# Performance work log

Measured on AMD Instinct MI355X. Metric: run time of the kernel, lower is better.

Reference implementation:

```python
import jax, jax.numpy as jnp
import numpy as np

H = 12            # heads
NB_FEATURES = 256 # Performer random features
EPS = 1e-4        # performer_pytorch softmax_kernel eps


def _gaussian_orthogonal_matrix(nb_rows, nb_cols, rng):
    # performer_pytorch gaussian_orthogonal_random_matrix, scaling=0
    nb_full = nb_rows // nb_cols
    blocks = []
    for _ in range(nb_full):
        q, _ = np.linalg.qr(rng.standard_normal((nb_cols, nb_cols)))
        blocks.append(q.T)
    rem = nb_rows - nb_full * nb_cols
    if rem > 0:
        q, _ = np.linalg.qr(rng.standard_normal((nb_cols, nb_cols)))
        blocks.append(q.T[:rem])
    M = np.concatenate(blocks, axis=0)
    multiplier = np.linalg.norm(rng.standard_normal((nb_rows, nb_cols)), axis=1)
    return (multiplier[:, None] * M).astype(np.float32)


def setup_inputs() -> dict:
    key = jax.random.key(0)
    ks = jax.random.split(key, 10)
    B, N, D = 8, 2048, 768
    s = D ** -0.5  # keep activations O(1) so exp() in FAVOR+ is stable
    inp = {
        "x": jax.random.normal(ks[0], (B, N, D), jnp.float32),
        "Wq": jax.random.normal(ks[1], (D, D), jnp.float32) * s,
        "bq": jnp.zeros((D,), jnp.float32),
        "Wk": jax.random.normal(ks[2], (D, D), jnp.float32) * s,
        "bk": jnp.zeros((D,), jnp.float32),
        "Wv": jax.random.normal(ks[3], (D, D), jnp.float32) * s,
        "bv": jnp.zeros((D,), jnp.float32),
        "Wo": jax.random.normal(ks[4], (D, D), jnp.float32) * s,
        "bo": jnp.zeros((D,), jnp.float32),
        "proj": jnp.asarray(_gaussian_orthogonal_matrix(NB_FEATURES, D // H, np.random.default_rng(0))),
    }
    return inp


def _softmax_kernel(x, proj, is_query):
    # x: [b,h,n,d], proj: [m,d] -> phi(x): [b,h,n,m]
    d = x.shape[-1]
    data_normalizer = d ** -0.25
    ratio = proj.shape[0] ** -0.5
    xp = jnp.einsum('bhnd,md->bhnm', x * data_normalizer, proj)
    diag = jnp.sum(x * x, axis=-1, keepdims=True) * 0.5 * (data_normalizer ** 2)
    if is_query:
        m = jax.lax.stop_gradient(jnp.max(xp, axis=-1, keepdims=True))
    else:
        m = jax.lax.stop_gradient(jnp.max(xp, axis=(-1, -2), keepdims=True))
    return ratio * (jnp.exp(xp - diag - m) + EPS)


def reference(x, Wq, bq, Wk, bk, Wv, bv, Wo, bo, proj):
    b, n, dim = x.shape
    d = dim // H
    # qkv projections, split into heads: [b,h,n,d]
    q = (x @ Wq.T + bq).reshape(b, n, H, d).transpose(0, 2, 1, 3)
    k = (x @ Wk.T + bk).reshape(b, n, H, d).transpose(0, 2, 1, 3)
    v = (x @ Wv.T + bv).reshape(b, n, H, d).transpose(0, 2, 1, 3)
    # FAVOR+ feature maps: [b,h,n,m]
    qp = _softmax_kernel(q, proj, True)
    kp = _softmax_kernel(k, proj, False)
    # non-causal linear attention
    k_sum = kp.sum(axis=2)                                  # [b,h,m]
    D_inv = 1.0 / jnp.einsum('bhnm,bhm->bhn', qp, k_sum)    # [b,h,n]
    ctx = jnp.einsum('bhnm,bhnd->bhmd', kp, v)              # [b,h,m,d]
    out = jnp.einsum('bhmd,bhnm,bhn->bhnd', ctx, qp, D_inv)
    out = out.transpose(0, 2, 1, 3).reshape(b, n, dim)
    return out @ Wo.T + bo
```

## Files before the change

kernel.cpp:

```cpp
#include <hip/hip_runtime.h>
#include <stdint.h>

typedef unsigned short u16;
typedef unsigned int u32;
typedef __attribute__((ext_vector_type(8))) short short8;
typedef __attribute__((ext_vector_type(4))) float floatx4;

#define HN 12
#define DH 64
#define DM 768
#define NS 2048
#define NB 8
#define MF 256
#define BN (NB*NS)
#define BH (NB*HN)

#define NRM 0.35355339059327373f
#define RATIO 0.0625f
#define EPSV 1e-4f

__device__ __forceinline__ float b2f(u32 u){ union{u32 i; float f;} x; x.i=u<<16; return x.f; }
__device__ __forceinline__ u32 f2b(float v){ union{float f; u32 u;} x; x.f=v; return (x.u + 0x7FFFu + ((x.u>>16)&1u))>>16; }
__device__ __forceinline__ u32 fkey(float v){ union{float f; u32 u;} x; x.f=v; return (x.u&0x80000000u)? ~x.u : (x.u|0x80000000u); }
__device__ __forceinline__ float funkey(u32 k){ union{u32 u; float f;} x; x.u=(k&0x80000000u)? (k^0x80000000u) : ~k; return x.f; }
__device__ __forceinline__ void bld8(uint4 r, float s, float* f){
  f[0]=b2f(r.x&0xffffu)*s; f[1]=b2f(r.x>>16)*s;
  f[2]=b2f(r.y&0xffffu)*s; f[3]=b2f(r.y>>16)*s;
  f[4]=b2f(r.z&0xffffu)*s; f[5]=b2f(r.z>>16)*s;
  f[6]=b2f(r.w&0xffffu)*s; f[7]=b2f(r.w>>16)*s;
}
__device__ __forceinline__ void load8(const void* base, size_t idx, int isf32, float s, float* f){
  if(isf32){
    const float* p=(const float*)base + idx;
    const float4 u=((const float4*)p)[0], v=((const float4*)p)[1];
    f[0]=u.x*s; f[1]=u.y*s; f[2]=u.z*s; f[3]=u.w*s;
    f[4]=v.x*s; f[5]=v.y*s; f[6]=v.z*s; f[7]=v.w*s;
  }else{
    uint4 r=*(const uint4*)((const u16*)base+idx);
    bld8(r,s,f);
  }
}
__device__ __forceinline__ float ld1(const void* base, int idx, int isf32){
  return isf32 ? ((const float*)base)[idx] : b2f((u32)((const u16*)base)[idx]);
}
__device__ __forceinline__ void gl16(const void* g, void* l){
  __builtin_amdgcn_global_load_lds(
    (const __attribute__((address_space(1))) u32*)g,
    (__attribute__((address_space(3))) u32*)l, 16, 0, 0);
}

__global__ __launch_bounds__(64) void k_detect(const u16* __restrict__ x, int* __restrict__ flag)
{
  __shared__ int w[64], z[64];
  const int t=threadIdx.x;
  int wild=0, zero=0;
  for(int i=t;i<256;i+=64){
    u32 u=(u32)x[2*i];
    u32 e=(u>>7)&0xFFu;
    if(e>=0x90u) wild++;
    if((u&0x7FFFu)==0u) zero++;
  }
  w[t]=wild; z[t]=zero; __syncthreads();
  if(t==0){
    int W=0,Z=0;
    for(int i=0;i<64;++i){W+=w[i];Z+=z[i];}
    flag[0]=(W>16||Z>200)?1:0;
  }
}

__global__ __launch_bounds__(256) void k_cvtw(const void* __restrict__ Wq,
    const void* __restrict__ Wk, const void* __restrict__ Wv, const void* __restrict__ Wo,
    u16* __restrict__ wb, u16* __restrict__ wob, const int* __restrict__ flagp)
{
  const int isf32=*flagp;
  const size_t WSZ=(size_t)DM*DM;
  size_t idx=((size_t)blockIdx.x*256+threadIdx.x)*8;
  const void* src; size_t off; u16* dst;
  if(idx<3*WSZ){ int w=(int)(idx/WSZ); src=(w==0)?Wq:((w==1)?Wk:Wv); off=idx-(size_t)w*WSZ; dst=wb+idx; }
  else { src=Wo; off=idx-3*WSZ; dst=wob+off; }
  if(isf32){
    const float* p=(const float*)src+off;
    float4 u=((const float4*)p)[0], v=((const float4*)p)[1];
    uint4 st;
    st.x=f2b(u.x)|(f2b(u.y)<<16); st.y=f2b(u.z)|(f2b(u.w)<<16);
    st.z=f2b(v.x)|(f2b(v.y)<<16); st.w=f2b(v.z)|(f2b(v.w)<<16);
    *(uint4*)dst=st;
  }else{
    *(uint4*)dst=*(const uint4*)((const u16*)src+off);
  }
}

__global__ __launch_bounds__(256) void k_cvtp(const void* __restrict__ proj,
    u16* __restrict__ pn, const int* __restrict__ flagp)
{
  const int isf32=*flagp;
  const size_t idx=((size_t)blockIdx.x*256+threadIdx.x)*8;
  float pf[8];
  load8(proj, idx, isf32, NRM, pf);
  uint4 st;
  st.x=f2b(pf[0])|(f2b(pf[1])<<16); st.y=f2b(pf[2])|(f2b(pf[3])<<16);
  st.z=f2b(pf[4])|(f2b(pf[5])<<16); st.w=f2b(pf[6])|(f2b(pf[7])<<16);
  *(uint4*)(pn+idx)=st;
}

__global__ __launch_bounds__(256) void k_cvtx(const void* __restrict__ x,
    u16* __restrict__ xb, const int* __restrict__ flagp)
{
  const int isf32=*flagp;
  const size_t idx=((size_t)blockIdx.x*256+threadIdx.x)*8;
  float f[8];
  load8(x, idx, isf32, 1.0f, f);
  uint4 st;
  st.x=f2b(f[0])|(f2b(f[1])<<16); st.y=f2b(f[2])|(f2b(f[3])<<16);
  st.z=f2b(f[4])|(f2b(f[5])<<16); st.w=f2b(f[6])|(f2b(f[7])<<16);
  *(uint4*)(xb+idx)=st;
}

__global__ __launch_bounds__(256) void k_diag(const u16* __restrict__ src, float* __restrict__ dk)
{
  const size_t row=(size_t)blockIdx.x*256+threadIdx.x;
  const u16* p=src+row*DH;
  float s=0.f;
#pragma unroll
  for(int c=0;c<DH;c+=8){
    uint4 r=*(const uint4*)(p+c);
    float f[8]; bld8(r,1.0f,f);
#pragma unroll
    for(int j=0;j<8;++j) s+=f[j]*f[j];
  }
  dk[row]=0.5f*NRM*NRM*s;
}

__device__ __forceinline__ void gemm_epilogue(const floatx4 acc[4][4], int mode, int oflag,
    int m0, int n0, int l, int wr4, int wc4,
    const void* bias0, const void* bias1, const void* bias2,
    u16* q, u16* k, u16* v, void* outv)
{
  const int rbase=(l>>4)*4, cl=l&15;
  if(mode==0){
    const int which=n0/DM;
    const void* bias=(which==0)?bias0:((which==1)?bias1:bias2);
    u16* outp=(which==0)?q:((which==1)?k:v);
    const int cb=n0-which*DM;
#pragma unroll
    for(int j=0;j<4;++j){
      const int col=cb+(wc4+j)*16+cl;
      const int h=col>>6, dd=col&63;
      const float bb=ld1(bias,col,oflag);
#pragma unroll
      for(int i=0;i<4;++i){
#pragma unroll
        for(int r=0;r<4;++r){
          const int grow=m0+(wr4+i)*16+rbase+r;
          const int b_=grow>>11, n=grow&2047;
          const u16 val=(u16)f2b(acc[i][j][r]+bb);
          if(which==2) outp[((size_t)(b_*HN+h)*DH+dd)*NS + n]=val;
          else         outp[((size_t)((b_*HN+h)*NS+n))*DH + dd]=val;
        }
      }
    }
  }else{
#pragma unroll
    for(int j=0;j<4;++j){
      const int col=n0+(wc4+j)*16+cl;
      const float bb=ld1(bias0,col,oflag);
#pragma unroll
      for(int i=0;i<4;++i){
#pragma unroll
        for(int r=0;r<4;++r){
          const int grow=m0+(wr4+i)*16+rbase+r;
          const float val=acc[i][j][r]+bb;
          if(oflag) ((float*)outv)[(size_t)grow*DM+col]=val;
          else      ((u16*)outv)[(size_t)grow*DM+col]=(u16)f2b(val);
        }
      }
    }
  }
}

__global__ __launch_bounds__(256) void k_gemm2(const u16* __restrict__ A16,
    const u16* __restrict__ B16,
    const void* __restrict__ bias0, const void* __restrict__ bias1, const void* __restrict__ bias2,
    u16* __restrict__ q, u16* __restrict__ k, u16* __restrict__ v,
    void* __restrict__ outv, const int* __restrict__ flagp, const int mode)
{
  __shared__ short At[16*512];
  __shared__ short Bt[16*512];
  const int oflag=*flagp;
  const int t=threadIdx.x, l=t&63, w=t>>6;
  const int m0=blockIdx.x*128, n0=blockIdx.y*128;
  const int wr4=(w>>1)*4, wc4=(w&1)*4;
  const int srow=l&15, skg=l>>4;
  floatx4 acc[4][4]={};
  for(int k0=0;k0<DM;k0+=64){
    __syncthreads();
#pragma unroll
    for(int s=0;s<4;++s){
      const int bi=w*4+s, rb=bi>>1, kh=bi&1;
      const int kc=k0+kh*32+skg*8;
      gl16(A16 + (size_t)(m0+rb*16+srow)*DM + kc, &At[bi*512]);
      gl16(B16 + (size_t)(n0+rb*16+srow)*DM + kc, &Bt[bi*512]);
    }
    __syncthreads();
#pragma unroll
    for(int kh=0;kh<2;++kh){
      short8 af[4], bf[4];
#pragma unroll
      for(int i=0;i<4;++i) af[i]=*(short8*)&At[((wr4+i)*2+kh)*512+l*8];
#pragma unroll
      for(int j=0;j<4;++j) bf[j]=*(short8*)&Bt[((wc4+j)*2+kh)*512+l*8];
#pragma unroll
      for(int i=0;i<4;++i)
#pragma unroll
        for(int j=0;j<4;++j)
          acc[i][j]=__builtin_amdgcn_mfma_f32_16x16x32_bf16(af[i],bf[j],acc[i][j],0,0,0);
    }
  }
  gemm_epilogue(acc,mode,oflag,m0,n0,l,wr4,wc4,bias0,bias1,bias2,q,k,v,outv);
}

__global__ __launch_bounds__(256) void k_gemm_f(const void* __restrict__ Araw,
    const u16* __restrict__ B16,
    const void* __restrict__ bias0, const void* __restrict__ bias1, const void* __restrict__ bias2,
    u16* __restrict__ q, u16* __restrict__ k, u16* __restrict__ v,
    void* __restrict__ outv, const int* __restrict__ flagp, const int mode)
{
  __shared__ short At[16*512];
  __shared__ short Bt[16*512];
  const int oflag=*flagp;
  const int isf32=(mode==0)?oflag:0;
  const int t=threadIdx.x, l=t&63, w=t>>6;
  const int m0=blockIdx.x*128, n0=blockIdx.y*128;
  const int wr4=(w>>1)*4, wc4=(w&1)*4;
  const int srow=l&15, skg=l>>4;
  floatx4 acc[4][4]={};
  for(int k0=0;k0<DM;k0+=64){
    __syncthreads();
#pragma unroll
    for(int s=0;s<4;++s){
      const int bi=w*4+s, rb=bi>>1, kh=bi&1;
      const int kc=k0+kh*32+skg*8;
      uint4 va;
      if(isf32){
        const float* ap=(const float*)Araw + (size_t)(m0+rb*16+srow)*DM + kc;
        float4 u=((const float4*)ap)[0], vv=((const float4*)ap)[1];
        va.x=f2b(u.x)|(f2b(u.y)<<16);  va.y=f2b(u.z)|(f2b(u.w)<<16);
        va.z=f2b(vv.x)|(f2b(vv.y)<<16); va.w=f2b(vv.z)|(f2b(vv.w)<<16);
      }else{
        va=*(const uint4*)((const u16*)Araw + (size_t)(m0+rb*16+srow)*DM + kc);
      }
      const uint4 vb=*(const uint4*)(B16 + (size_t)(n0+rb*16+srow)*DM + kc);
      *(uint4*)&At[bi*512+l*8]=va;
      *(uint4*)&Bt[bi*512+l*8]=vb;
    }
    __syncthreads();
#pragma unroll
    for(int kh=0;kh<2;++kh){
      short8 af[4], bf[4];
#pragma unroll
      for(int i=0;i<4;++i) af[i]=*(short8*)&At[((wr4+i)*2+kh)*512+l*8];
#pragma unroll
      for(int j=0;j<4;++j) bf[j]=*(short8*)&Bt[((wc4+j)*2+kh)*512+l*8];
#pragma unroll
      for(int i=0;i<4;++i)
#pragma unroll
        for(int j=0;j<4;++j)
          acc[i][j]=__builtin_amdgcn_mfma_f32_16x16x32_bf16(af[i],bf[j],acc[i][j],0,0,0);
    }
  }
  gemm_epilogue(acc,mode,oflag,m0,n0,l,wr4,wc4,bias0,bias1,bias2,q,k,v,outv);
}

#define G9OFF(s,u) (((s)*24+(u))*512)
#define G9STA(kt,s) do{ \
  const size_t g_=(size_t)(kt)*32; \
  gl16(Ar0+g_, &LD[G9OFF(s,w)]); \
  gl16(Ar0+(size_t)128*768+g_, &LD[G9OFF(s,8+w)]); \
  gl16(Br0+g_, &LD[G9OFF(s,16+w)]); \
}while(0)
#define G9LD(s) do{ \
  _Pragma("unroll") for(int i_=0;i_<4;++i_) a[i_]=*(short8*)&LD[G9OFF(s,wr4+i_)+l*8]; \
  _Pragma("unroll") for(int j_=0;j_<4;++j_) b[j_]=*(short8*)&LD[G9OFF(s,16+wc4+j_)+l*8]; \
}while(0)
#define G9MM do{ _Pragma("unroll") for(int i_=0;i_<4;++i_){ \
  _Pragma("unroll") for(int j_=0;j_<4;++j_) \
    acc[i_][j_]=__builtin_amdgcn_mfma_f32_16x16x32_bf16(a[i_],b[j_],acc[i_][j_],0,0,0); } }while(0)
#define FEN asm volatile("" ::: "memory")
#define BARR do{ FEN; __builtin_amdgcn_s_barrier(); FEN; }while(0)
#define WV3 asm volatile("s_waitcnt vmcnt(3)" ::: "memory")
#define WV0 asm volatile("s_waitcnt vmcnt(0)" ::: "memory")
#define WL0 do{ asm volatile("s_waitcnt lgkmcnt(0)" ::: "memory"); __builtin_amdgcn_sched_barrier(0); }while(0)
#define G9PH(kt,s,SST,WST) do{ G9LD(s); SST; WST; BARR; WL0; \
  __builtin_amdgcn_s_setprio(1); G9MM; __builtin_amdgcn_s_setprio(0); BARR; }while(0)

__global__ __launch_bounds__(512,4) void k_gemm9(const u16* __restrict__ A16,
    const u16* __restrict__ B16,
    const void* __restrict__ bias0, const void* __restrict__ bias1, const void* __restrict__ bias2,
    u16* __restrict__ q, u16* __restrict__ k, u16* __restrict__ v,
    void* __restrict__ outv, const int* __restrict__ flagp, const int mode,
    float* __restrict__ dq_, float* __restrict__ dk_)
{
  __shared__ short LD[3*24*512];
  const int oflag=*flagp;
  const int t=threadIdx.x, l=t&63, w=t>>6;
  const int wr=w>>1, wc=w&1;
  const int wr4=wr*4, wc4=wc*4;
  const int lrow=l&15, lk8=(l>>4)*8;
  int bid = blockIdx.y*gridDim.x + blockIdx.x;
  const int nwg = gridDim.x*gridDim.y;
  const int nN  = gridDim.y;
  bid = (bid&7)*(nwg>>3) + (bid>>3);
  const int mi = bid/nN;
  const int m0 = mi*256;
  const int n0 = (bid - mi*nN)*128;

  const u16* Ar0 = A16 + (size_t)(m0 + w*16 + lrow)*768 + lk8;
  const u16* Br0 = B16 + (size_t)(n0 + w*16 + lrow)*768 + lk8;
  floatx4 acc[4][4]={};
  short8 a[4], b[4];

  G9STA(0,0); G9STA(1,1);
  WV3; BARR;

  for(int it=0; it<7; ++it){
    const int kt=3*it;
    G9PH(kt+0,0, G9STA(kt+2,2), WV3);
    G9PH(kt+1,1, G9STA(kt+3,0), WV3);
    G9PH(kt+2,2, G9STA(kt+4,1), WV3);
  }
  G9PH(21,0, G9STA(23,2), WV3);
  G9PH(22,1, (void)0, WV0);
  G9PH(23,2, (void)0, (void)0);

  char* LB=(char*)LD;
  const int cl=l&15, q4=l>>4;
  const int wrm=wr*64, wcn=wc*64;
  if(mode==0){
    const int which=n0/DM;
    const int cb0=n0-which*DM;
    const int hb=cb0>>6;
    const void* bias=(which==0)?bias0:((which==1)?bias1:bias2);
    u16* outp=(which==0)?q:((which==1)?k:v);
    if(which==2){
#pragma unroll
      for(int j=0;j<4;++j){
        const int col=wcn+j*16+cl;
        const float bb=ld1(bias,cb0+col,oflag);
        const int X=(col&7)<<4;
#pragma unroll
        for(int i=0;i<4;++i){
          const int rowb=wrm+i*16+q4*4;
          uint2 pk;
          pk.x=f2b(acc[i][j][0]+bb)|(f2b(acc[i][j][1]+bb)<<16);
          pk.y=f2b(acc[i][j][2]+bb)|(f2b(acc[i][j][3]+bb)<<16);
          *(uint2*)(LB + col*512 + ((rowb*2)^X)) = pk;
        }
      }
      __syncthreads();
      const int b_=m0>>11, nbase=m0&2047;
#pragma unroll
      for(int s8=0;s8<8;++s8){
        const int c=s8*512+t;
        const int col=c>>5, off=(c&31)*16;
        const uint4 d4=*(const uint4*)(LB + col*512 + (off^((col&7)<<4)));
        const int h=hb+(col>>6), dd=col&63;
        *(uint4*)&outp[((size_t)(b_*HN+h)*DH+dd)*NS + nbase + (off>>1)]=d4;
      }
    } else {
      float bb4[4];
#pragma unroll
      for(int j=0;j<4;++j) bb4[j]=ld1(bias, cb0+wcn+j*16+cl, oflag);
      float* dptr=(which==0)? dq_ : dk_;
#pragma unroll
      for(int i=0;i<4;++i){
#pragma unroll
        for(int r=0;r<4;++r){
          const int row=wrm+i*16+q4*4+r;
          const int X=(row&7)<<4;
          float s=0.f;
#pragma unroll
          for(int j=0;j<4;++j){
            const int col=wcn+j*16+cl;
            const u16 hv=(u16)f2b(acc[i][j][r]+bb4[j]);
            *(u16*)(LB + row*256 + ((col*2)^X)) = hv;
            const float fv=b2f(hv);
            s+=fv*fv;
          }
          s+=__shfl_xor(s,1,64); s+=__shfl_xor(s,2,64);
          s+=__shfl_xor(s,4,64); s+=__shfl_xor(s,8,64);
          if(cl==0){
            const int grow=m0+row, b_=grow>>11, n=grow&2047;
            dptr[(size_t)(b_*HN + hb + wc)*NS + n]=0.5f*NRM*NRM*s;
          }
        }
      }
      __syncthreads();
#pragma unroll
      for(int s8=0;s8<8;++s8){
        const int c=s8*512+t;
        const int row=c>>4, off=(c&15)*16;
        const uint4 d4=*(const uint4*)(LB + row*256 + (off^((row&7)<<4)));
        const int grow=m0+row, b_=grow>>11, n=grow&2047;
        *(uint4*)&outp[((size_t)((b_*HN+hb+(off>>7))*NS+n))*DH + ((off>>1)&63)]=d4;
      }
    }
  } else {
    if(oflag){
#pragma unroll
      for(int p=0;p<2;++p){
        if((wr>>1)==p){
          const int rl0=(wr&1)*64;
#pragma unroll
          for(int j=0;j<4;++j){
            const int col=wcn+j*16+cl;
            const float bb=ld1(bias0,n0+col,oflag);
#pragma unroll
            for(int i=0;i<4;++i){
#pragma unroll
              for(int r=0;r<4;++r){
                const int rl=rl0+i*16+q4*4+r;
                *(float*)(LB + rl*512 + ((col*4)^((rl&7)<<4))) = acc[i][j][r]+bb;
              }
            }
          }
        }
        __syncthreads();
#pragma unroll
        for(int s8=0;s8<8;++s8){
          const int c=s8*512+t;
          const int rl=c>>5, off=(c&31)*16;
          const uint4 d4=*(const uint4*)(LB + rl*512 + (off^((rl&7)<<4)));
          const size_t grow=(size_t)m0+p*128+rl;
          *(uint4*)((char*)outv + (grow*DM+n0)*4 + off)=d4;
        }
        __syncthreads();
      }
    } else {
#pragma unroll
      for(int j=0;j<4;++j){
        const int col=wcn+j*16+cl;
        const float bb=ld1(bias0,n0+col,oflag);
#pragma unroll
        for(int i=0;i<4;++i){
#pragma unroll
          for(int r=0;r<4;++r){
            const int row=wrm+i*16+q4*4+r;
            *(u16*)(LB + row*256 + ((col*2)^((row&7)<<4))) = (u16)f2b(acc[i][j][r]+bb);
          }
        }
      }
      __syncthreads();
#pragma unroll
      for(int s8=0;s8<8;++s8){
        const int c=s8*512+t;
        const int row=c>>4, off=(c&15)*16;
        const uint4 d4=*(const uint4*)(LB + row*256 + (off^((row&7)<<4)));
        *(uint4*)((u16*)outv + (size_t)(m0+row)*DM + n0 + (off>>1))=d4;
      }
    }
  }
}

__global__ __launch_bounds__(256) void k_xpk2(const u16* __restrict__ kb,
    const u16* __restrict__ pn, u32* __restrict__ kmax)
{
  __shared__ short Bt[32*512];
  __shared__ short At[8*512];
  __shared__ float red[256];
  const int t=threadIdx.x, l=t&63, w=t>>6;
  const int bh=blockIdx.y, nb0=blockIdx.x*256;
  for(int s=t;s<2048;s+=256){
    const int ub=s>>6, l2=s&63, mt=ub>>1, kh=ub&1;
    const int row=mt*16+(l2&15), kc=kh*32+(l2>>4)*8;
    *(uint4*)&Bt[ub*512+l2*8]=*(const uint4*)(pn + (size_t)row*DH + kc);
  }
  float vmax=-3.4e38f;
  for(int c=0;c<4;++c){
    const int n0=nb0+c*64;
    __syncthreads();
    for(int s=t;s<512;s+=256){
      const int ua=s>>6, l2=s&63, rb=ua>>1, kh=ua&1;
      const int n=n0+rb*16+(l2&15), kc=kh*32+(l2>>4)*8;
      *(uint4*)&At[ua*512+l2*8]=*(const uint4*)(kb + ((size_t)bh*NS+n)*DH + kc);
    }
    __syncthreads();
    const short8 af0=*(short8*)&At[(w*2+0)*512+l*8];
    const short8 af1=*(short8*)&At[(w*2+1)*512+l*8];
#pragma unroll
    for(int mt=0;mt<16;++mt){
      floatx4 a={};
      a=__builtin_amdgcn_mfma_f32_16x16x32_bf16(af0,*(short8*)&Bt[(mt*2+0)*512+l*8],a,0,0,0);
      a=__builtin_amdgcn_mfma_f32_16x16x32_bf16(af1,*(short8*)&Bt[(mt*2+1)*512+l*8],a,0,0,0);
      vmax=fmaxf(vmax,fmaxf(fmaxf(a[0],a[1]),fmaxf(a[2],a[3])));
    }
  }
  red[t]=vmax; __syncthreads();
  for(int s=128;s>0;s>>=1){ if(t<s) red[t]=fmaxf(red[t],red[t+s]); __syncthreads(); }
  if(t==0) atomicMax(kmax+bh, fkey(red[0]));
}

__global__ __launch_bounds__(256) void k_ctx2(const u16* __restrict__ kb,
    const u16* __restrict__ vT, const u16* __restrict__ pn,
    const float* __restrict__ dkbuf, const u32* __restrict__ kmax,
    float* __restrict__ ctxT, float* __restrict__ ksum)
{
  __shared__ short Bt[32*512];
  __shared__ u16   Ks[256*72];
  __shared__ short AtV[8*512];
  __shared__ float dg[64];
  const int t=threadIdx.x, l=t&63, w=t>>6;
  const int split=blockIdx.x, bh=blockIdx.y;
  for(int s=t;s<2048;s+=256){
    const int ub=s>>6, l2=s&63, mt=ub>>1, kh=ub&1;
    const int row=mt*16+(l2&15), kc=kh*32+(l2>>4)*8;
    *(uint4*)&Bt[ub*512+l2*8]=*(const uint4*)(pn + (size_t)row*DH + kc);
  }
  const float kM=funkey(kmax[bh]);
  float ksr=0.f;
  floatx4 acc2[4][4]={};
  for(int c=0;c<8;++c){
    const int n0=split*512+c*64;
    __syncthreads();
    for(int s=t;s<512;s+=256){
      const int ua=s>>6, l2=s&63, rb=ua>>1, kh=ua&1;
      const int n=n0+rb*16+(l2&15), kc=kh*32+(l2>>4)*8;
      *(uint4*)&AtV[ua*512+l2*8]=*(const uint4*)(kb + ((size_t)bh*NS+n)*DH + kc);
    }
    if(t<64) dg[t]=dkbuf[(size_t)bh*NS+n0+t];
    __syncthreads();
    short8 af[4][2];
#pragma unroll
    for(int rb=0;rb<4;++rb){
      af[rb][0]=*(short8*)&AtV[(rb*2+0)*512+l*8];
      af[rb][1]=*(short8*)&AtV[(rb*2+1)*512+l*8];
    }
    float dgl[16];
#pragma unroll
    for(int rb=0;rb<4;++rb)
#pragma unroll
      for(int r=0;r<4;++r) dgl[rb*4+r]=dg[rb*16+(l>>4)*4+r];
#pragma unroll
    for(int ml=0;ml<4;++ml){
      const int mt=w*4+ml;
      const short8 bf0=*(short8*)&Bt[(mt*2+0)*512+l*8];
      const short8 bf1=*(short8*)&Bt[(mt*2+1)*512+l*8];
      const int m=mt*16+(l&15);
#pragma unroll
      for(int rb=0;rb<4;++rb){
        floatx4 a={};
        a=__builtin_amdgcn_mfma_f32_16x16x32_bf16(af[rb][0],bf0,a,0,0,0);
        a=__builtin_amdgcn_mfma_f32_16x16x32_bf16(af[rb][1],bf1,a,0,0,0);
        const int nb=rb*16+(l>>4)*4;
        const float v0=RATIO*(__expf(a[0]-dgl[rb*4+0]-kM)+EPSV);
        const float v1=RATIO*(__expf(a[1]-dgl[rb*4+1]-kM)+EPSV);
        const float v2=RATIO*(__expf(a[2]-dgl[rb*4+2]-kM)+EPSV);
        const float v3=RATIO*(__expf(a[3]-dgl[rb*4+3]-kM)+EPSV);
        *(u32*)&Ks[m*72+nb]  =f2b(v0)|(f2b(v1)<<16);
        *(u32*)&Ks[m*72+nb+2]=f2b(v2)|(f2b(v3)<<16);
      }
    }
    __syncthreads();
    for(int s=t;s<512;s+=256){
      const int uv=s>>6, l2=s&63, dt=uv>>1, kh=uv&1;
      const int d=dt*16+(l2&15), nn=n0+kh*32+(l2>>4)*8;
      *(uint4*)&AtV[uv*512+l2*8]=*(const uint4*)(vT + ((size_t)bh*DH+d)*NS + nn);
    }
    {
      float s8=0.f;
#pragma unroll
      for(int j=0;j<8;++j){
        const uint4 kk=*(const uint4*)&Ks[t*72+j*8];
        s8+=b2f(kk.x&0xffffu)+b2f(kk.x>>16)+b2f(kk.y&0xffffu)+b2f(kk.y>>16)
           +b2f(kk.z&0xffffu)+b2f(kk.z>>16)+b2f(kk.w&0xffffu)+b2f(kk.w>>16);
      }
      ksr+=s8;
    }
    __syncthreads();
#pragma unroll
    for(int i=0;i<4;++i){
      const int row=(w*4+i)*16+(l&15);
      const short8 a0=*(short8*)&Ks[row*72 + 0*32+(l>>4)*8];
      const short8 a1=*(short8*)&Ks[row*72 + 1*32+(l>>4)*8];
#pragma unroll
      for(int dt=0;dt<4;++dt){
        acc2[i][dt]=__builtin_amdgcn_mfma_f32_16x16x32_bf16(a0,*(short8*)&AtV[(dt*2+0)*512+l*8],acc2[i][dt],0,0,0);
        acc2[i][dt]=__builtin_amdgcn_mfma_f32_16x16x32_bf16(a1,*(short8*)&AtV[(dt*2+1)*512+l*8],acc2[i][dt],0,0,0);
      }
    }
  }
#pragma unroll
  for(int i=0;i<4;++i){
#pragma unroll
    for(int dt=0;dt<4;++dt){
#pragma unroll
      for(int r=0;r<4;++r){
        const int m=(w*4+i)*16+(l>>4)*4+r;
        const int d=dt*16+(l&15);
        atomicAdd(&ctxT[((size_t)bh*DH+d)*MF+m], acc2[i][dt][r]);
      }
    }
  }
  atomicAdd(ksum+bh*MF+t, ksr);
}

__global__ __launch_bounds__(256,2) void k_ctx3(const u16* __restrict__ kb,
    const u16* __restrict__ vT, const u16* __restrict__ pn,
    const float* __restrict__ dkbuf, const u32* __restrict__ kmax,
    float* __restrict__ ctxP, float* __restrict__ ksumP)
{
  __shared__ __align__(16) char SM[66048];
  short* Ks=(short*)SM;
  short* Kb=(short*)(SM+32768);
  short* Vb=(short*)(SM+49152);
  float* dgb=(float*)(SM+65536);
  const int t=threadIdx.x, l=t&63, w=t>>6;
  const int split=blockIdx.x, bh=blockIdx.y;
  const int n00=split*512;
  const int lrow=l&15, lk8=(l>>4)*8;
  const u16* kbase = kb + (size_t)bh*NS*DH;
  const u16* vbase = vT + (size_t)bh*DH*NS;
  short8 bf[4][2];
#pragma unroll
  for(int ml=0;ml<4;++ml)
#pragma unroll
    for(int kh=0;kh<2;++kh)
      bf[ml][kh]=*(const short8*)(pn + (size_t)((w*4+ml)*16+lrow)*DH + kh*32 + lk8);
  const float kM=funkey(kmax[bh]);
  {
#pragma unroll
    for(int p=0;p<2;++p){
      const int u=w+4*p, rb=u>>1, kh=u&1;
      gl16(kbase + (size_t)(n00+rb*16+lrow)*DH + kh*32+lk8, &Kb[u*512]);
    }
#pragma unroll
    for(int p=0;p<2;++p){
      const int u=w+4*p, dt=u>>1, kh=u&1;
      gl16(vbase + (size_t)(dt*16+lrow)*NS + n00+kh*32+lk8, &Vb[u*512]);
    }
    if(t<64) dgb[t]=dkbuf[(size_t)bh*NS+n00+t];
  }
  __syncthreads();
  float ksr=0.f;
  floatx4 acc2[4][4]={};
  for(int c=0;c<8;++c){
    const int cur=c&1, nxt=cur^1;
    if(c<7){
      const int n1=n00+(c+1)*64;
#pragma unroll
      for(int p=0;p<2;++p){
        const int u=w+4*p, rb=u>>1, kh=u&1;
        gl16(kbase + (size_t)(n1+rb*16+lrow)*DH + kh*32+lk8, &Kb[nxt*4096+u*512]);
      }
#pragma unroll
      for(int p=0;p<2;++p){
        const int u=w+4*p, dt=u>>1, kh=u&1;
        gl16(vbase + (size_t)(dt*16+lrow)*NS + n1+kh*32+lk8, &Vb[nxt*4096+u*512]);
      }
    }
    float dgnv=0.f;
    if(c<7 && t<64) dgnv=dkbuf[(size_t)bh*NS+n00+(c+1)*64+t];
    short8 af[4][2];
#pragma unroll
    for(int rb=0;rb<4;++rb){
      af[rb][0]=*(short8*)&Kb[cur*4096+(rb*2+0)*512+l*8];
      af[rb][1]=*(short8*)&Kb[cur*4096+(rb*2+1)*512+l*8];
    }
    float dgl[16];
#pragma unroll
    for(int rb=0;rb<4;++rb){
      const float4 dv=*(const float4*)&dgb[cur*64+rb*16+(l>>4)*4];
      dgl[rb*4+0]=dv.x; dgl[rb*4+1]=dv.y; dgl[rb*4+2]=dv.z; dgl[rb*4+3]=dv.w;
    }
#pragma unroll
    for(int ml=0;ml<4;++ml){
      const int m=(w*4+ml)*16+lrow;
      char* krow=(char*)Ks + m*128;
      const int xr=(m&7)<<4;
#pragma unroll
      for(int rb=0;rb<4;++rb){
        floatx4 a={};
        a=__builtin_amdgcn_mfma_f32_16x16x32_bf16(af[rb][0],bf[ml][0],a,0,0,0);
        a=__builtin_amdgcn_mfma_f32_16x16x32_bf16(af[rb][1],bf[ml][1],a,0,0,0);
        const float v0=RATIO*(__expf(a[0]-dgl[rb*4+0]-kM)+EPSV);
        const float v1=RATIO*(__expf(a[1]-dgl[rb*4+1]-kM)+EPSV);
        const float v2=RATIO*(__expf(a[2]-dgl[rb*4+2]-kM)+EPSV);
        const float v3=RATIO*(__expf(a[3]-dgl[rb*4+3]-kM)+EPSV);
        const int nb=rb*16+(l>>4)*4;
        const u32 bo=((u32)(nb*2)) ^ xr;
        *(u32*)(krow+bo)  =f2b(v0)|(f2b(v1)<<16);
        *(u32*)(krow+bo+4)=f2b(v2)|(f2b(v3)<<16);
      }
    }
    __syncthreads();
    {
      char* krow=(char*)Ks + t*128;
      const int xr=(t&7)<<4;
      float s8=0.f;
#pragma unroll
      for(int j=0;j<8;++j){
        const uint4 kk=*(const uint4*)(krow + ((j*16)^xr));
        s8+=b2f(kk.x&0xffffu)+b2f(kk.x>>16)+b2f(kk.y&0xffffu)+b2f(kk.y>>16)
           +b2f(kk.z&0xffffu)+b2f(kk.z>>16)+b2f(kk.w&0xffffu)+b2f(kk.w>>16);
      }
      ksr+=s8;
    }
#pragma unroll
    for(int i=0;i<4;++i){
      const int row=(w*4+i)*16+lrow;
      char* krow=(char*)Ks + row*128;
      const int xr=(row&7)<<4;
      const short8 a0=*(short8*)(krow + (((l>>4)*16)^xr));
      const short8 a1=*(short8*)(krow + ((64+(l>>4)*16)^xr));
#pragma unroll
      for(int dt=0;dt<4;++dt){
        acc2[i][dt]=__builtin_amdgcn_mfma_f32_16x16x32_bf16(a0,*(short8*)&Vb[cur*4096+(dt*2+0)*512+l*8],acc2[i][dt],0,0,0);
        acc2[i][dt]=__builtin_amdgcn_mfma_f32_16x16x32_bf16(a1,*(short8*)&Vb[cur*4096+(dt*2+1)*512+l*8],acc2[i][dt],0,0,0);
      }
    }
    if(c<7 && t<64) dgb[nxt*64+t]=dgnv;
    __syncthreads();
  }
  {
    float* OUT=(float*)SM;
#pragma unroll
    for(int i=0;i<4;++i){
      const int mb=(w*4+i)*16+(l>>4)*4;
#pragma unroll
      for(int dt=0;dt<4;++dt){
        const int d=dt*16+lrow;
        float4 o; o.x=acc2[i][dt][0]; o.y=acc2[i][dt][1]; o.z=acc2[i][dt][2]; o.w=acc2[i][dt][3];
        *(float4*)((char*)OUT + d*1024 + ((mb*4)^((d&15)<<4))) = o;
      }
    }
    __syncthreads();
    float* gout = ctxP + (size_t)(split*BH+bh)*64*256;
#pragma unroll
    for(int s=0;s<16;++s){
      const int d=s*4+w;
      const uint4 o4=*(const uint4*)((char*)OUT + d*1024 + ((l*16)^((d&15)<<4)));
      *(uint4*)(gout + (size_t)d*256 + l*4)=o4;
    }
    ksumP[(size_t)(split*BH+bh)*256 + t]=ksr;
  }
}

__global__ __launch_bounds__(256) void k_csplit(const float* __restrict__ ctxT,
    u16* __restrict__ chi, u16* __restrict__ clo, float* __restrict__ ecs)
{
  __shared__ float cred[256];
  const int bh=blockIdx.x, t=threadIdx.x;
  const int d=t>>2, part=t&3;
  const size_t base=((size_t)bh*DH+d)*MF + part*64;
  const float* src=ctxT + base;
  u16* ph=chi + base;
  u16* pl=clo + base;
  float cs=0.f;
  for(int m=0;m<64;m+=4){
    float4 v=*(const float4*)(src+m);
    float vv[4]={v.x,v.y,v.z,v.w};
    u32 h_[4], l_[4];
#pragma unroll
    for(int j=0;j<4;++j){
      cs+=vv[j];
      u32 hh=f2b(vv[j]);
      float rr=vv[j]-b2f(hh);
      h_[j]=hh; l_[j]=f2b(rr);
    }
    uint2 sh, sl;
    sh.x=h_[0]|(h_[1]<<16); sh.y=h_[2]|(h_[3]<<16);
    sl.x=l_[0]|(l_[1]<<16); sl.y=l_[2]|(l_[3]<<16);
    *(uint2*)(ph+m)=sh; *(uint2*)(pl+m)=sl;
  }
  cred[t]=cs; __syncthreads();
  if(part==0) ecs[bh*64+d]=EPSV*(cred[t]+cred[t+1]+cred[t+2]+cred[t+3]);
}

__global__ __launch_bounds__(256) void k_csplit3(const float* __restrict__ ctxP,
    const float* __restrict__ ksumP,
    u16* __restrict__ chi, u16* __restrict__ clo, float* __restrict__ ecs,
    float* __restrict__ ksum)
{
  __shared__ float wred[16][4];
  const int bh=blockIdx.y, dq=blockIdx.x;
  const int t=threadIdx.x, l=t&63, w=t>>6;
  if(dq==0){
    float kv=0.f;
#pragma unroll
    for(int s=0;s<4;++s) kv+=ksumP[(size_t)(s*BH+bh)*256+t];
    ksum[bh*MF+t]=kv;
  }
#pragma unroll
  for(int d16=0;d16<16;++d16){
    const int d=dq*16+d16;
    float v=0.f;
#pragma unroll
    for(int s=0;s<4;++s) v+=ctxP[((size_t)(s*BH+bh)*64+d)*256+t];
    const u32 hh=f2b(v);
    const float rr=v-b2f(hh);
    const size_t ob=((size_t)bh*DH+d)*MF+t;
    chi[ob]=(u16)hh; clo[ob]=(u16)f2b(rr);
    float s_=v;
    s_+=__shfl_xor(s_,1,64); s_+=__shfl_xor(s_,2,64); s_+=__shfl_xor(s_,4,64);
    s_+=__shfl_xor(s_,8,64); s_+=__shfl_xor(s_,16,64); s_+=__shfl_xor(s_,32,64);
    if(l==0) wred[d16][w]=s_;
  }
  __syncthreads();
  if(t<16) ecs[bh*64+dq*16+t]=EPSV*(wred[t][0]+wred[t][1]+wred[t][2]+wred[t][3]);
}

__global__ __launch_bounds__(256) void k_attn2(const u16* __restrict__ qb,
    const u16* __restrict__ pn, const float* __restrict__ dqbuf,
    const float* __restrict__ ksum, const u16* __restrict__ chi, const u16* __restrict__ clo,
    const float* __restrict__ ecs, u16* __restrict__ attn)
{
  __shared__ short At[8*512];
  __shared__ u16 Qf[32*512];
  __shared__ float ksums[256];
  __shared__ float dq_s[64];
  __shared__ float mxs[4][64];
  __shared__ float s1s[4][64];
  __shared__ float a_s[64], dinv_s[64], ec_s[64];
  __shared__ float red4[4];
  __shared__ float epkss;
  const int t=threadIdx.x, l=t&63, w=t>>6;
  const int bh=blockIdx.y, nb0=blockIdx.x*256;
  const int b_=bh/HN, h=bh%HN;
  {
    float kv=ksum[bh*MF+t];
    ksums[t]=kv;
    if(t<64) ec_s[t]=ecs[bh*64+t];
    float s=kv;
#pragma unroll
    for(int o=1;o<64;o<<=1) s+=__shfl_xor(s,o,64);
    if(l==0) red4[w]=s;
  }
  __syncthreads();
  if(t==0) epkss=EPSV*(red4[0]+red4[1]+red4[2]+red4[3]);
  short8 bhf[8], blf[8];
  {
    const int d=w*16+(l&15);
    const size_t base=((size_t)bh*DH+d)*MF;
#pragma unroll
    for(int kc=0;kc<8;++kc){
      const size_t off=base + kc*32+(l>>4)*8;
      bhf[kc]=*(const short8*)(chi+off);
      blf[kc]=*(const short8*)(clo+off);
    }
  }
  for(int c=0;c<4;++c){
    const int n0c=nb0+c*64;
    __syncthreads();
    for(int s=t;s<512;s+=256){
      const int ua=s>>6, l2=s&63, nt=ua>>1, kh=ua&1;
      const int n=n0c+nt*16+(l2&15), kc=kh*32+(l2>>4)*8;
      *(uint4*)&At[ua*512+l2*8]=*(const uint4*)(qb + ((size_t)bh*NS+n)*DH + kc);
    }
    if(t<64) dq_s[t]=dqbuf[(size_t)bh*NS+n0c+t];
    __syncthreads();
    float mxl[4]={-3.4e38f,-3.4e38f,-3.4e38f,-3.4e38f};
    float s1l[4]={0.f,0.f,0.f,0.f};
#pragma unroll
    for(int mt=0;mt<4;++mt){
      const int gm=w*4+mt;
      const u16* pr=pn + ((gm*16+(l&15))<<6) + (l>>4)*8;
      const short8 a0=*(const short8*)(pr);
      const short8 a1=*(const short8*)(pr+32);
      float k4[4];
#pragma unroll
      for(int r=0;r<4;++r) k4[r]=ksums[gm*16+(l>>4)*4+r];
      const int mbase=(gm&1)*16+(l>>4)*4;
      const int lane2=((mbase>>3)*16+(l&15))*8 + (mbase&7);
#pragma unroll
      for(int nt=0;nt<4;++nt){
        floatx4 xp={};
        xp=__builtin_amdgcn_mfma_f32_16x16x32_bf16(a0,*(short8*)&At[(nt*2+0)*512+l*8],xp,0,0,0);
        xp=__builtin_amdgcn_mfma_f32_16x16x32_bf16(a1,*(short8*)&At[(nt*2+1)*512+l*8],xp,0,0,0);
        const float dq=dq_s[nt*16+(l&15)];
        float ev[4];
#pragma unroll
        for(int r=0;r<4;++r){
          const float xv=xp[r];
          mxl[nt]=fmaxf(mxl[nt],xv);
          ev[r]=__expf(xv-dq);
          s1l[nt]+=ev[r]*k4[r];
        }
        u16* qp_=&Qf[(nt*8+(gm>>1))*512 + lane2];
        *(u32*)qp_    =f2b(ev[0])|(f2b(ev[1])<<16);
        *(u32*)(qp_+2)=f2b(ev[2])|(f2b(ev[3])<<16);
      }
    }
#pragma unroll
    for(int nt=0;nt<4;++nt){
      float m_=mxl[nt], s_=s1l[nt];
      m_=fmaxf(m_,__shfl_xor(m_,16,64)); s_+=__shfl_xor(s_,16,64);
      m_=fmaxf(m_,__shfl_xor(m_,32,64)); s_+=__shfl_xor(s_,32,64);
      if(l<16){ mxs[w][nt*16+l]=m_; s1s[w][nt*16+l]=s_; }
    }
    __syncthreads();
    if(t<64){
      float m_=fmaxf(fmaxf(mxs[0][t],mxs[1][t]),fmaxf(mxs[2][t],mxs[3][t]));
      float s_=s1s[0][t]+s1s[1][t]+s1s[2][t]+s1s[3][t];
      float a=__expf(-m_);
      a_s[t]=a;
      dinv_s[t]=1.0f/(a*s_+epkss);
    }
    __syncthreads();
    const int d=w*16+(l&15);
    const float ec=ec_s[d];
#pragma unroll
    for(int nt=0;nt<4;++nt){
      floatx4 y={};
#pragma unroll
      for(int kc=0;kc<8;++kc){
        const short8 e=*(short8*)&Qf[(nt*8+kc)*512+l*8];
        y=__builtin_amdgcn_mfma_f32_16x16x32_bf16(e,bhf[kc],y,0,0,0);
        y=__builtin_amdgcn_mfma_f32_16x16x32_bf16(e,blf[kc],y,0,0,0);
      }
#pragma unroll
      for(int r=0;r<4;++r){
        const int nl=nt*16+(l>>4)*4+r;
        const float val=(a_s[nl]*y[r]+ec)*dinv_s[nl];
        attn[((size_t)(b_*NS+n0c+nl))*DM + h*DH + d]=(u16)f2b(val);
      }
    }
  }
}

extern "C" void kernel_launch(void* const* d_in, const int* in_sizes, int n_in,
                              void* d_out, int out_size, void* d_ws, size_t ws_size,
                              hipStream_t stream)
{
  (void)in_sizes; (void)n_in; (void)out_size;
  const void* x =d_in[0];
  const void* Wq=d_in[1]; const void* bq=d_in[2];
  const void* Wk=d_in[3]; const void* bk=d_in[4];
  const void* Wv=d_in[5]; const void* bv=d_in[6];
  const void* Wo=d_in[7]; const void* bo=d_in[8];
  const void* proj=d_in[9];

  char* ws=(char*)d_ws;
  const size_t SZ=(size_t)BN*DM*2;
  const size_t AUXSZ=19030528;
  const bool big = ws_size >= 4*SZ + AUXSZ;
  u16*   qb  =(u16*)(ws);
  u16*   kb  =(u16*)(ws+SZ);
  u16*   vb  =(u16*)(ws+2*SZ);
  u16*   xb  =(u16*)(ws+3*SZ);
  char*  aux = big ? (ws+4*SZ) : (ws+3*SZ);
  u16*   wb   =(u16*)(aux);
  u16*   wob  =(u16*)(aux+3538944);
  float* ctxT =(float*)(aux+4718592);
  float* ksum =(float*)(aux+11010048);
  u32*   kmax =(u32*)(aux+11108352);
  int*   flag =(int*)(aux+11108736);
  float* dk   =(float*)(aux+11108864);
  float* dqq  =(float*)(aux+11895296);
  u16*   pn   =(u16*)(aux+12681728);
  u16*   chi  =(u16*)(aux+12714496);
  u16*   clo  =(u16*)(aux+15860224);
  float* ecs  =(float*)(aux+19005952);
  u16*   attnb = big ? xb : kb;

  k_detect<<<1,64,0,stream>>>((const u16*)x, flag);
  if(big) hipMemsetAsync(kmax, 0, 384, stream);
  else    hipMemsetAsync(ctxT, 0, 6291456+98304+384, stream);
  k_cvtw <<<1152, 256, 0, stream>>>(Wq,Wk,Wv,Wo,wb,wob,flag);
  k_cvtp <<<8, 256, 0, stream>>>(proj, pn, flag);
  if(big){
    k_cvtx <<<(BN*DM)/2048, 256, 0, stream>>>(x, xb, flag);
    k_gemm9<<<dim3(64,18), 512, 0, stream>>>(xb, wb, bq,bk,bv, qb,kb,vb, nullptr, flag, 0, dqq, dk);
  }else{
    k_gemm_f<<<dim3(BN/128,2304/128), 256, 0, stream>>>(x, wb, bq,bk,bv, qb,kb,vb, nullptr, flag, 0);
    k_diag <<<(BH*NS)/256, 256, 0, stream>>>(kb, dk);
    k_diag <<<(BH*NS)/256, 256, 0, stream>>>(qb, dqq);
  }
  k_xpk2 <<<dim3(NS/256,BH), 256, 0, stream>>>(kb, pn, kmax);
  if(big){
    float* ctxP =(float*)xb;
    float* ksumP=ctxT;
    k_ctx3 <<<dim3(4,BH), 256, 0, stream>>>(kb, vb, pn, dk, kmax, ctxP, ksumP);
    k_csplit3<<<dim3(4,BH), 256, 0, stream>>>(ctxP, ksumP, chi, clo, ecs, ksum);
  }else{
    k_ctx2 <<<dim3(4,BH), 256, 0, stream>>>(kb, vb, pn, dk, kmax, ctxT, ksum);
    k_csplit<<<BH, 256, 0, stream>>>(ctxT, chi, clo, ecs);
  }
  k_attn2<<<dim3(NS/256,BH), 256, 0, stream>>>(qb, pn, dqq, ksum, chi, clo, ecs, attnb);
  if(big){
    k_gemm9<<<dim3(64,6), 512, 0, stream>>>(attnb, wob, bo,bo,bo, nullptr,nullptr,nullptr, d_out, flag, 1, nullptr, nullptr);
  }else{
    k_gemm2<<<dim3(BN/128,DM/128), 256, 0, stream>>>(attnb, wob, bo,bo,bo, nullptr,nullptr,nullptr, d_out, flag, 1);
  }
}
```

Measured before the change: 397.3 us.

## Switch GEMM to double-buffered LDS and split epilogue to raise occupancy

The k_gemm9 main loop drops from a three-stage LDS ring to a two-stage double buffer, cutting shared memory from 72KB to 48KB, and launch bounds move from 4 to 6 blocks per CU. To fit the smaller LDS, every epilogue path (V transpose, Q/K with norm sums, fp32 and bf16 output) now stages its output through LDS in two or four sequential halves, with extra barriers. The goal is more resident waves to hide latency, at the cost of a shallower prefetch, an added barrier per k-step, and tighter register limits that could cause spills.

```diff
diff --git a/kernel.cpp b/kernel.cpp
--- a/kernel.cpp
+++ b/kernel.cpp
@@ -271,18 +271,18 @@
   gemm_epilogue(acc,mode,oflag,m0,n0,l,wr4,wc4,bias0,bias1,bias2,q,k,v,outv);
 }
 
-#define G9OFF(s,u) (((s)*24+(u))*512)
-#define G9STA(kt,s) do{ \
+#define GAOFF(s,u) (((s)*24+(u))*512)
+#define GASTA(kt,s) do{ \
   const size_t g_=(size_t)(kt)*32; \
-  gl16(Ar0+g_, &LD[G9OFF(s,w)]); \
-  gl16(Ar0+(size_t)128*768+g_, &LD[G9OFF(s,8+w)]); \
-  gl16(Br0+g_, &LD[G9OFF(s,16+w)]); \
+  gl16(Ar0+g_, &LD[GAOFF(s,w)]); \
+  gl16(Ar0+(size_t)128*768+g_, &LD[GAOFF(s,8+w)]); \
+  gl16(Br0+g_, &LD[GAOFF(s,16+w)]); \
 }while(0)
-#define G9LD(s) do{ \
-  _Pragma("unroll") for(int i_=0;i_<4;++i_) a[i_]=*(short8*)&LD[G9OFF(s,wr4+i_)+l*8]; \
-  _Pragma("unroll") for(int j_=0;j_<4;++j_) b[j_]=*(short8*)&LD[G9OFF(s,16+wc4+j_)+l*8]; \
+#define GALD(s) do{ \
+  _Pragma("unroll") for(int i_=0;i_<4;++i_) a[i_]=*(short8*)&LD[GAOFF(s,wr4+i_)+l*8]; \
+  _Pragma("unroll") for(int j_=0;j_<4;++j_) b[j_]=*(short8*)&LD[GAOFF(s,16+wc4+j_)+l*8]; \
 }while(0)
-#define G9MM do{ _Pragma("unroll") for(int i_=0;i_<4;++i_){ \
+#define GAMM do{ _Pragma("unroll") for(int i_=0;i_<4;++i_){ \
   _Pragma("unroll") for(int j_=0;j_<4;++j_) \
     acc[i_][j_]=__builtin_amdgcn_mfma_f32_16x16x32_bf16(a[i_],b[j_],acc[i_][j_],0,0,0); } }while(0)
 #define FEN asm volatile("" ::: "memory")
@@ -290,17 +290,16 @@
 #define WV3 asm volatile("s_waitcnt vmcnt(3)" ::: "memory")
 #define WV0 asm volatile("s_waitcnt vmcnt(0)" ::: "memory")
 #define WL0 do{ asm volatile("s_waitcnt lgkmcnt(0)" ::: "memory"); __builtin_amdgcn_sched_barrier(0); }while(0)
-#define G9PH(kt,s,SST,WST) do{ G9LD(s); SST; WST; BARR; WL0; \
-  __builtin_amdgcn_s_setprio(1); G9MM; __builtin_amdgcn_s_setprio(0); BARR; }while(0)
-
-__global__ __launch_bounds__(512,4) void k_gemm9(const u16* __restrict__ A16,
+#define GACOMP do{ WL0; __builtin_amdgcn_s_setprio(1); GAMM; __builtin_amdgcn_s_setprio(0); }while(0)
+
+__global__ __launch_bounds__(512,6) void k_gemm9(const u16* __restrict__ A16,
     const u16* __restrict__ B16,
     const void* __restrict__ bias0, const void* __restrict__ bias1, const void* __restrict__ bias2,
     u16* __restrict__ q, u16* __restrict__ k, u16* __restrict__ v,
     void* __restrict__ outv, const int* __restrict__ flagp, const int mode,
     float* __restrict__ dq_, float* __restrict__ dk_)
 {
-  __shared__ short LD[3*24*512];
+  __shared__ short LD[2*24*512];
   const int oflag=*flagp;
   const int t=threadIdx.x, l=t&63, w=t>>6;
   const int wr=w>>1, wc=w&1;
@@ -319,18 +318,20 @@
   floatx4 acc[4][4]={};
   short8 a[4], b[4];
 
-  G9STA(0,0); G9STA(1,1);
+  GASTA(0,0); GASTA(1,1);
   WV3; BARR;
 
-  for(int it=0; it<7; ++it){
-    const int kt=3*it;
-    G9PH(kt+0,0, G9STA(kt+2,2), WV3);
-    G9PH(kt+1,1, G9STA(kt+3,0), WV3);
-    G9PH(kt+2,2, G9STA(kt+4,1), WV3);
-  }
-  G9PH(21,0, G9STA(23,2), WV3);
-  G9PH(22,1, (void)0, WV0);
-  G9PH(23,2, (void)0, (void)0);
+  for(int tt=0; tt<22; ++tt){
+    const int sl=tt&1;
+    GALD(sl);
+    GACOMP;
+    BARR;
+    GASTA(tt+2,sl);
+    WV3;
+    BARR;
+  }
+  GALD(0); GACOMP; BARR; WV0; BARR;
+  GALD(1); GACOMP; BARR;
 
   char* LB=(char*)LD;
   const int cl=l&15, q4=l>>4;
@@ -342,75 +343,86 @@
     const void* bias=(which==0)?bias0:((which==1)?bias1:bias2);
     u16* outp=(which==0)?q:((which==1)?k:v);
     if(which==2){
-#pragma unroll
-      for(int j=0;j<4;++j){
-        const int col=wcn+j*16+cl;
-        const float bb=ld1(bias,cb0+col,oflag);
-        const int X=(col&7)<<4;
-#pragma unroll
-        for(int i=0;i<4;++i){
-          const int rowb=wrm+i*16+q4*4;
-          uint2 pk;
-          pk.x=f2b(acc[i][j][0]+bb)|(f2b(acc[i][j][1]+bb)<<16);
-          pk.y=f2b(acc[i][j][2]+bb)|(f2b(acc[i][j][3]+bb)<<16);
-          *(uint2*)(LB + col*512 + ((rowb*2)^X)) = pk;
+      const int b_=m0>>11, nbase=m0&2047;
+#pragma unroll
+      for(int p=0;p<2;++p){
+        if(wc==p){
+#pragma unroll
+          for(int j=0;j<4;++j){
+            const int clc=j*16+cl;
+            const float bb=ld1(bias,cb0+p*64+clc,oflag);
+            const int X=(clc&7)<<4;
+#pragma unroll
+            for(int i=0;i<4;++i){
+              const int rowb=wrm+i*16+q4*4;
+              uint2 pk;
+              pk.x=f2b(acc[i][j][0]+bb)|(f2b(acc[i][j][1]+bb)<<16);
+              pk.y=f2b(acc[i][j][2]+bb)|(f2b(acc[i][j][3]+bb)<<16);
+              *(uint2*)(LB + clc*512 + ((rowb*2)^X)) = pk;
+            }
+          }
         }
-      }
-      __syncthreads();
-      const int b_=m0>>11, nbase=m0&2047;
-#pragma unroll
-      for(int s8=0;s8<8;++s8){
-        const int c=s8*512+t;
-        const int col=c>>5, off=(c&31)*16;
-        const uint4 d4=*(const uint4*)(LB + col*512 + (off^((col&7)<<4)));
-        const int h=hb+(col>>6), dd=col&63;
-        *(uint4*)&outp[((size_t)(b_*HN+h)*DH+dd)*NS + nbase + (off>>1)]=d4;
+        __syncthreads();
+#pragma unroll
+        for(int s8=0;s8<4;++s8){
+          const int c=s8*512+t;
+          const int clc=c>>5, off=(c&31)*16;
+          const uint4 d4=*(const uint4*)(LB + clc*512 + (off^((clc&7)<<4)));
+          *(uint4*)&outp[((size_t)(b_*HN+hb+p)*DH+clc)*NS + nbase + (off>>1)]=d4;
+        }
+        __syncthreads();
       }
     } else {
       float bb4[4];
 #pragma unroll
       for(int j=0;j<4;++j) bb4[j]=ld1(bias, cb0+wcn+j*16+cl, oflag);
       float* dptr=(which==0)? dq_ : dk_;
-#pragma unroll
-      for(int i=0;i<4;++i){
-#pragma unroll
-        for(int r=0;r<4;++r){
-          const int row=wrm+i*16+q4*4+r;
-          const int X=(row&7)<<4;
-          float s=0.f;
-#pragma unroll
-          for(int j=0;j<4;++j){
-            const int col=wcn+j*16+cl;
-            const u16 hv=(u16)f2b(acc[i][j][r]+bb4[j]);
-            *(u16*)(LB + row*256 + ((col*2)^X)) = hv;
-            const float fv=b2f(hv);
-            s+=fv*fv;
-          }
-          s+=__shfl_xor(s,1,64); s+=__shfl_xor(s,2,64);
-          s+=__shfl_xor(s,4,64); s+=__shfl_xor(s,8,64);
-          if(cl==0){
-            const int grow=m0+row, b_=grow>>11, n=grow&2047;
-            dptr[(size_t)(b_*HN + hb + wc)*NS + n]=0.5f*NRM*NRM*s;
-          }
-        }
-      }
-      __syncthreads();
-#pragma unroll
-      for(int s8=0;s8<8;++s8){
-        const int c=s8*512+t;
-        const int row=c>>4, off=(c&15)*16;
-        const uint4 d4=*(const uint4*)(LB + row*256 + (off^((row&7)<<4)));
-        const int grow=m0+row, b_=grow>>11, n=grow&2047;
-        *(uint4*)&outp[((size_t)((b_*HN+hb+(off>>7))*NS+n))*DH + ((off>>1)&63)]=d4;
-      }
-    }
-  } else {
-    if(oflag){
 #pragma unroll
       for(int p=0;p<2;++p){
         if((wr>>1)==p){
           const int rl0=(wr&1)*64;
 #pragma unroll
+          for(int i=0;i<4;++i){
+#pragma unroll
+            for(int r=0;r<4;++r){
+              const int rl=rl0+i*16+q4*4+r;
+              const int X=(rl&7)<<4;
+              float s=0.f;
+#pragma unroll
+              for(int j=0;j<4;++j){
+                const int col=wcn+j*16+cl;
+                const u16 hv=(u16)f2b(acc[i][j][r]+bb4[j]);
+                *(u16*)(LB + rl*256 + ((col*2)^X)) = hv;
+                const float fv=b2f(hv);
+                s+=fv*fv;
+              }
+              s+=__shfl_xor(s,1,64); s+=__shfl_xor(s,2,64);
+              s+=__shfl_xor(s,4,64); s+=__shfl_xor(s,8,64);
+              if(cl==0){
+                const int grow=m0+p*128+rl, b_=grow>>11, n=grow&2047;
+                dptr[(size_t)(b_*HN + hb + wc)*NS + n]=0.5f*NRM*NRM*s;
+              }
+            }
+          }
+        }
+        __syncthreads();
+#pragma unroll
+        for(int s8=0;s8<4;++s8){
+          const int c=s8*512+t;
+          const int row=c>>4, off=(c&15)*16;
+          const uint4 d4=*(const uint4*)(LB + row*256 + (off^((row&7)<<4)));
+          const int grow=m0+p*128+row, b_=grow>>11, n=grow&2047;
+          *(uint4*)&outp[((size_t)((b_*HN+hb+(off>>7))*NS+n))*DH + ((off>>1)&63)]=d4;
+        }
+        __syncthreads();
+      }
+    }
+  } else {
+    if(oflag){
+#pragma unroll
+      for(int p=0;p<4;++p){
+        if(wr==p){
+#pragma unroll
           for(int j=0;j<4;++j){
             const int col=wcn+j*16+cl;
             const float bb=ld1(bias0,n0+col,oflag);
@@ -418,7 +430,7 @@
             for(int i=0;i<4;++i){
 #pragma unroll
               for(int r=0;r<4;++r){
-                const int rl=rl0+i*16+q4*4+r;
+                const int rl=i*16+q4*4+r;
                 *(float*)(LB + rl*512 + ((col*4)^((rl&7)<<4))) = acc[i][j][r]+bb;
               }
             }
@@ -426,36 +438,43 @@
         }
         __syncthreads();
 #pragma unroll
-        for(int s8=0;s8<8;++s8){
+        for(int s8=0;s8<4;++s8){
           const int c=s8*512+t;
           const int rl=c>>5, off=(c&31)*16;
           const uint4 d4=*(const uint4*)(LB + rl*512 + (off^((rl&7)<<4)));
-          const size_t grow=(size_t)m0+p*128+rl;
+          const size_t grow=(size_t)m0+p*64+rl;
           *(uint4*)((char*)outv + (grow*DM+n0)*4 + off)=d4;
         }
         __syncthreads();
       }
     } else {
 #pragma unroll
-      for(int j=0;j<4;++j){
-        const int col=wcn+j*16+cl;
-        const float bb=ld1(bias0,n0+col,oflag);
-#pragma unroll
-        for(int i=0;i<4;++i){
-#pragma unroll
-          for(int r=0;r<4;++r){
-            const int row=wrm+i*16+q4*4+r;
-            *(u16*)(LB + row*256 + ((col*2)^((row&7)<<4))) = (u16)f2b(acc[i][j][r]+bb);
+      for(int p=0;p<2;++p){
+        if((wr>>1)==p){
+          const int rl0=(wr&1)*64;
+#pragma unroll
+          for(int j=0;j<4;++j){
+            const int col=wcn+j*16+cl;
+            const float bb=ld1(bias0,n0+col,oflag);
+#pragma unroll
+            for(int i=0;i<4;++i){
+#pragma unroll
+              for(int r=0;r<4;++r){
+                const int rl=rl0+i*16+q4*4+r;
+                *(u16*)(LB + rl*256 + ((col*2)^((rl&7)<<4))) = (u16)f2b(acc[i][j][r]+bb);
+              }
+            }
           }
         }
-      }
-      __syncthreads();
-#pragma unroll
-      for(int s8=0;s8<8;++s8){
-        const int c=s8*512+t;
-        const int row=c>>4, off=(c&15)*16;
-        const uint4 d4=*(const uint4*)(LB + row*256 + (off^((row&7)<<4)));
-        *(uint4*)((u16*)outv + (size_t)(m0+row)*DM + n0 + (off>>1))=d4;
+        __syncthreads();
+#pragma unroll
+        for(int s8=0;s8<4;++s8){
+          const int c=s8*512+t;
+          const int row=c>>4, off=(c&15)*16;
+          const uint4 d4=*(const uint4*)(LB + row*256 + (off^((row&7)<<4)));
+          *(uint4*)((u16*)outv + (size_t)(m0+p*128+row)*DM + n0 + (off>>1))=d4;
+        }
+        __syncthreads();
       }
     }
   }
```

Measured after the change: 1.279 ms. 3.22x slower.
